# Kernel tuning notes

Hardware: AMD Instinct MI355X
Metric: run time of the kernel (lower is better)

Reference implementation:

```python
import jax, jax.numpy as jnp
import numpy as np

ALPHA = 0.2        # LeakyReLU slope
NEG_BIG = -9e15    # mask fill value from the original module


def setup_inputs() -> dict:
    key = jax.random.key(0)
    k1, k2, k3, k4 = jax.random.split(key, 4)
    N, F_IN, F_OUT = 8192, 256, 128
    h = jax.random.normal(k1, (N, F_IN), dtype=jnp.float32)
    adj = jax.random.randint(k2, (N, N), 0, 2, dtype=jnp.int32)
    W = jax.random.normal(k3, (F_IN, F_OUT), dtype=jnp.float32) * (1.0 / np.sqrt(F_IN))
    a = jax.random.normal(k4, (2 * F_OUT, 1), dtype=jnp.float32) * (1.0 / np.sqrt(2 * F_OUT))
    return {"h": h, "adj": adj, "W": W, "a": a}


def reference(h, adj, W, a):
    f_out = W.shape[1]
    Wh = h @ W                                   # [N, F_out]
    Wh1 = Wh @ a[:f_out, :]                      # [N, 1]
    Wh2 = Wh @ a[f_out:, :]                      # [N, 1]
    e = Wh1 + Wh2.T                              # [N, N] broadcast-add
    e = jnp.where(e > 0, e, ALPHA * e)           # LeakyReLU
    e = jnp.where(adj > 0, e, NEG_BIG)           # adjacency mask
    attention = jax.nn.softmax(e, axis=-1)       # row softmax
    # dropout rate = 0.0 -> identity
    h_prime = attention @ Wh                     # [N, F_out]
    return jax.nn.elu(h_prime)
```

## Files before the change

### kernel.cpp

```cpp
#include <hip/hip_runtime.h>

#define NV 8192
#define FIN 256
#define FOUT 128
#define NSPLIT 8
#define SPLITW 1024

typedef __bf16 bf16_t;
typedef __attribute__((ext_vector_type(8))) __bf16 bf16x8;
typedef __attribute__((ext_vector_type(16))) float f32x16;

__global__ __launch_bounds__(256) void wh_kernel(
    const float* __restrict__ h, const float* __restrict__ W,
    const float* __restrict__ a,
    bf16_t* __restrict__ WhbT,
    float* __restrict__ E1, float* __restrict__ F1,
    float* __restrict__ E2, float* __restrict__ F2)
{
  __shared__ float As[64][34];
  __shared__ float Bs[64][128];
  __shared__ float Cs[32][129];
  __shared__ float red1[32][16];
  __shared__ float red2[32][16];
  const int t  = threadIdx.x;
  const int i0 = blockIdx.x * 32;
  const int c  = t & 15;
  const int r  = t >> 4;
  float acc0[8], acc1[8];
  #pragma unroll
  for (int j = 0; j < 8; j++) { acc0[j] = 0.f; acc1[j] = 0.f; }

  for (int k0 = 0; k0 < FIN; k0 += 64) {
    {
      const int ia = t >> 3;
      const int ka = (t & 7) * 8;
      const float* src = h + (size_t)(i0 + ia) * FIN + k0 + ka;
      float4 v0 = *(const float4*)src;
      float4 v1 = *(const float4*)(src + 4);
      As[ka+0][ia]=v0.x; As[ka+1][ia]=v0.y; As[ka+2][ia]=v0.z; As[ka+3][ia]=v0.w;
      As[ka+4][ia]=v1.x; As[ka+5][ia]=v1.y; As[ka+6][ia]=v1.z; As[ka+7][ia]=v1.w;
    }
    {
      const int kb = t >> 2;
      const int cb = (t & 3) * 32;
      const float4* src = (const float4*)(W + (size_t)(k0 + kb) * FOUT + cb);
      float4* dst = (float4*)&Bs[kb][cb];
      #pragma unroll
      for (int q = 0; q < 8; q++) dst[q] = src[q];
    }
    __syncthreads();
    #pragma unroll 4
    for (int k = 0; k < 64; k++) {
      float2 av = *(const float2*)&As[k][r*2];
      float b[8];
      *(float4*)&b[0] = *(const float4*)&Bs[k][c*8];
      *(float4*)&b[4] = *(const float4*)&Bs[k][c*8+4];
      #pragma unroll
      for (int j = 0; j < 8; j++) {
        acc0[j] = fmaf(av.x, b[j], acc0[j]);
        acc1[j] = fmaf(av.y, b[j], acc1[j]);
      }
    }
    __syncthreads();
  }

  float p1a = 0.f, p2a = 0.f, p1b = 0.f, p2b = 0.f;
  #pragma unroll
  for (int j = 0; j < 8; j++) {
    Cs[r*2][c*8+j]   = acc0[j];
    Cs[r*2+1][c*8+j] = acc1[j];
    float w1 = a[c*8+j];
    float w2 = a[FOUT + c*8+j];
    p1a = fmaf(acc0[j], w1, p1a); p2a = fmaf(acc0[j], w2, p2a);
    p1b = fmaf(acc1[j], w1, p1b); p2b = fmaf(acc1[j], w2, p2b);
  }
  red1[r*2][c]   = p1a; red2[r*2][c]   = p2a;
  red1[r*2+1][c] = p1b; red2[r*2+1][c] = p2b;
  __syncthreads();
  if (t < 32) {
    float s = 0.f;
    #pragma unroll
    for (int q = 0; q < 16; q++) s += red1[t][q];
    E1[i0 + t] = __expf(s);
    F1[i0 + t] = __expf(0.2f * s);
  } else if (t < 64) {
    float s = 0.f;
    #pragma unroll
    for (int q = 0; q < 16; q++) s += red2[t-32][q];
    E2[i0 + t - 32] = __expf(s);
    F2[i0 + t - 32] = __expf(0.2f * s);
  }
  {
    const int f = t & 127, half = t >> 7;
    union { bf16_t b[16]; uint4 v[2]; } pk;
    #pragma unroll
    for (int q = 0; q < 16; q++) pk.b[q] = (bf16_t)Cs[half*16 + q][f];
    uint4* dst = (uint4*)(WhbT + (size_t)f * NV + i0 + half*16);
    dst[0] = pk.v[0]; dst[1] = pk.v[1];
  }
}

__global__ __launch_bounds__(256, 4) void attn_kernel(
    const int* __restrict__ adj, const bf16_t* __restrict__ WhbT,
    const float* __restrict__ E1v, const float* __restrict__ F1v,
    const float* __restrict__ E2v, const float* __restrict__ F2v,
    float* __restrict__ nump, float* __restrict__ denp)
{
  __shared__ bf16_t Plds[64][72];
  __shared__ bf16_t Blds[128][72];
  __shared__ float denlds[64][4];
  const int t     = threadIdx.x;
  const int rb    = blockIdx.x >> 3;
  const int split = blockIdx.x & 7;
  const int i0 = rb * 64;
  const int j0 = split * SPLITW;
  const int il = t >> 2;
  const int jg = (t & 3) * 16;
  const float e1 = E1v[i0 + il];
  const float f1 = F1v[i0 + il];
  const int lane = t & 63;
  const int w    = t >> 6;
  const int rh = (w & 1) * 32;
  const int ch = (w >> 1) * 64;
  const int ml = lane & 31;
  const int kh = (lane >> 5) * 8;
  f32x16 acc0 = {};
  f32x16 acc1 = {};
  float den_t = 0.f;

  const int* arow = adj + (size_t)(i0 + il) * NV + j0 + jg;
  int4 ca0 = *(const int4*)(arow + 0);
  int4 ca1 = *(const int4*)(arow + 4);
  int4 ca2 = *(const int4*)(arow + 8);
  int4 ca3 = *(const int4*)(arow + 12);

  for (int jc = 0; jc < SPLITW; jc += 64) {
    const int jb = j0 + jc;
    const int jn = (jc + 64 < SPLITW) ? jc + 64 : jc;
    const int* nrow = arow + jn;
    int4 na0 = *(const int4*)(nrow + 0);
    int4 na1 = *(const int4*)(nrow + 4);
    int4 na2 = *(const int4*)(nrow + 8);
    int4 na3 = *(const int4*)(nrow + 12);
    {
      const int n  = t >> 1;
      const int hf = (t & 1) * 32;
      const uint4* s4 = (const uint4*)(WhbT + (size_t)n * NV + jb + hf);
      uint4* dst = (uint4*)&Blds[n][hf];
      dst[0] = s4[0]; dst[1] = s4[1]; dst[2] = s4[2]; dst[3] = s4[3];
    }
    {
      const float* e2p = E2v + jb + jg;
      const float* f2p = F2v + jb + jg;
      union { bf16_t b[16]; bf16x8 v[2]; } pk;
      float d0 = 0.f, d1 = 0.f, d2 = 0.f, d3 = 0.f;
      #define PGRP(CA, GG, DD) { \
        float4 e4 = *(const float4*)(e2p + 4*GG); \
        float4 f4 = *(const float4*)(f2p + 4*GG); \
        float px = fmaxf(e1*e4.x, f1*f4.x); px = (CA.x > 0) ? px : 0.f; DD += px; pk.b[4*GG+0] = (bf16_t)px; \
        float py = fmaxf(e1*e4.y, f1*f4.y); py = (CA.y > 0) ? py : 0.f; DD += py; pk.b[4*GG+1] = (bf16_t)py; \
        float pz = fmaxf(e1*e4.z, f1*f4.z); pz = (CA.z > 0) ? pz : 0.f; DD += pz; pk.b[4*GG+2] = (bf16_t)pz; \
        float pw = fmaxf(e1*e4.w, f1*f4.w); pw = (CA.w > 0) ? pw : 0.f; DD += pw; pk.b[4*GG+3] = (bf16_t)pw; }
      PGRP(ca0, 0, d0)
      PGRP(ca1, 1, d1)
      PGRP(ca2, 2, d2)
      PGRP(ca3, 3, d3)
      #undef PGRP
      den_t += (d0 + d1) + (d2 + d3);
      *(bf16x8*)&Plds[il][jg]     = pk.v[0];
      *(bf16x8*)&Plds[il][jg + 8] = pk.v[1];
    }
    asm volatile("s_waitcnt lgkmcnt(0)\n\ts_barrier" ::: "memory");
    #pragma unroll
    for (int ks = 0; ks < 4; ks++) {
      const int k = ks * 16 + kh;
      bf16x8 af = *(const bf16x8*)&Plds[rh + ml][k];
      bf16x8 b0 = *(const bf16x8*)&Blds[ch + ml][k];
      bf16x8 b1 = *(const bf16x8*)&Blds[ch + 32 + ml][k];
      acc0 = __builtin_amdgcn_mfma_f32_32x32x16_bf16(af, b0, acc0, 0, 0, 0);
      acc1 = __builtin_amdgcn_mfma_f32_32x32x16_bf16(af, b1, acc1, 0, 0, 0);
    }
    __syncthreads();
    ca0 = na0; ca1 = na1; ca2 = na2; ca3 = na3;
  }

  denlds[il][t & 3] = den_t;
  __syncthreads();
  if (t < 64) {
    denp[(size_t)split * NV + i0 + t] =
        denlds[t][0] + denlds[t][1] + denlds[t][2] + denlds[t][3];
  }
  float* base = nump + ((size_t)split * NV + i0) * FOUT;
  const int col = ch + ml;
  const int r4  = 4 * (lane >> 5);
  #pragma unroll
  for (int reg = 0; reg < 16; reg++) {
    const int row = rh + (reg & 3) + 8 * (reg >> 2) + r4;
    base[(size_t)row * FOUT + col]      = acc0[reg];
    base[(size_t)row * FOUT + col + 32] = acc1[reg];
  }
}

__global__ __launch_bounds__(256) void finalize_kernel(
    const float* __restrict__ nump, const float* __restrict__ denp,
    float* __restrict__ out)
{
  const int gid = blockIdx.x * 256 + threadIdx.x;
  const int i  = gid >> 5;
  const int f0 = (gid & 31) * 4;
  float den = 0.f;
  #pragma unroll
  for (int sp = 0; sp < NSPLIT; sp++) den += denp[(size_t)sp * NV + i];
  float4 s = make_float4(0.f, 0.f, 0.f, 0.f);
  #pragma unroll
  for (int sp = 0; sp < NSPLIT; sp++) {
    float4 v = *(const float4*)&nump[((size_t)sp * NV + i) * FOUT + f0];
    s.x += v.x; s.y += v.y; s.z += v.z; s.w += v.w;
  }
  const float inv = 1.0f / den;
  float4 r;
  r.x = s.x * inv; r.y = s.y * inv; r.z = s.z * inv; r.w = s.w * inv;
  r.x = r.x > 0.f ? r.x : __expf(r.x) - 1.0f;
  r.y = r.y > 0.f ? r.y : __expf(r.y) - 1.0f;
  r.z = r.z > 0.f ? r.z : __expf(r.z) - 1.0f;
  r.w = r.w > 0.f ? r.w : __expf(r.w) - 1.0f;
  *(float4*)&out[(size_t)i * FOUT + f0] = r;
}

extern "C" void kernel_launch(void* const* d_in, const int* in_sizes, int n_in,
                              void* d_out, int out_size, void* d_ws, size_t ws_size,
                              hipStream_t stream) {
  const float* h  = (const float*)d_in[0];
  const int*  adj = (const int*)d_in[1];
  const float* W  = (const float*)d_in[2];
  const float* a  = (const float*)d_in[3];
  float* out = (float*)d_out;
  char* ws = (char*)d_ws;
  bf16_t* WhbT = (bf16_t*)ws;
  float* E1   = (float*)(ws + 2097152);
  float* F1   = (float*)(ws + 2129920);
  float* E2   = (float*)(ws + 2162688);
  float* F2   = (float*)(ws + 2195456);
  float* denp = (float*)(ws + 2228224);
  float* nump = (float*)(ws + 2490368);

  wh_kernel<<<256, 256, 0, stream>>>(h, W, a, WhbT, E1, F1, E2, F2);
  attn_kernel<<<1024, 256, 0, stream>>>(adj, WhbT, E1, F1, E2, F2, nump, denp);
  finalize_kernel<<<1024, 256, 0, stream>>>(nump, denp, out);
}
```

Before: 414.0 us.

## Prefetch Wh tile into registers and double-buffer its shared-memory copy

The attention kernel now loads the next chunk's WhbT slice into registers during the current iteration and writes it into one of two shared-memory buffers, so the global load latency overlaps the MFMA work. The E2/F2 loads are hoisted ahead of the compute, and the trailing __syncthreads is replaced by a bare s_barrier. The extra buffer raises shared-memory use and register pressure, so the occupancy hint drops from 4 to 3 blocks per CU. Dropping the full waitcnt before the barrier relies on the double buffer to stay correct.

```diff
diff --git a/kernel.cpp b/kernel.cpp
--- a/kernel.cpp
+++ b/kernel.cpp
@@ -100,14 +100,14 @@
   }
 }
 
-__global__ __launch_bounds__(256, 4) void attn_kernel(
+__global__ __launch_bounds__(256, 3) void attn_kernel(
     const int* __restrict__ adj, const bf16_t* __restrict__ WhbT,
     const float* __restrict__ E1v, const float* __restrict__ F1v,
     const float* __restrict__ E2v, const float* __restrict__ F2v,
     float* __restrict__ nump, float* __restrict__ denp)
 {
   __shared__ bf16_t Plds[64][72];
-  __shared__ bf16_t Blds[128][72];
+  __shared__ bf16_t Blds[2][128][72];
   __shared__ float denlds[64][4];
   const int t     = threadIdx.x;
   const int rb    = blockIdx.x >> 3;
@@ -128,59 +128,74 @@
   f32x16 acc1 = {};
   float den_t = 0.f;
 
+  const int bn  = t >> 1;
+  const int bhf = (t & 1) * 32;
+  const bf16_t* bsrc = WhbT + (size_t)bn * NV + j0 + bhf;
   const int* arow = adj + (size_t)(i0 + il) * NV + j0 + jg;
+
+  uint4 br0, br1, br2, br3;
+  {
+    const uint4* s4 = (const uint4*)bsrc;
+    br0 = s4[0]; br1 = s4[1]; br2 = s4[2]; br3 = s4[3];
+  }
   int4 ca0 = *(const int4*)(arow + 0);
   int4 ca1 = *(const int4*)(arow + 4);
   int4 ca2 = *(const int4*)(arow + 8);
   int4 ca3 = *(const int4*)(arow + 12);
 
   for (int jc = 0; jc < SPLITW; jc += 64) {
-    const int jb = j0 + jc;
+    const int jb  = j0 + jc;
+    const int buf = (jc >> 6) & 1;
+    {
+      uint4* bd = (uint4*)&Blds[buf][bn][bhf];
+      bd[0] = br0; bd[1] = br1; bd[2] = br2; bd[3] = br3;
+    }
+    float4 w0 = *(const float4*)(E2v + jb + jg);
+    float4 w1 = *(const float4*)(E2v + jb + jg + 4);
+    float4 w2 = *(const float4*)(E2v + jb + jg + 8);
+    float4 w3 = *(const float4*)(E2v + jb + jg + 12);
+    float4 x0 = *(const float4*)(F2v + jb + jg);
+    float4 x1 = *(const float4*)(F2v + jb + jg + 4);
+    float4 x2 = *(const float4*)(F2v + jb + jg + 8);
+    float4 x3 = *(const float4*)(F2v + jb + jg + 12);
     const int jn = (jc + 64 < SPLITW) ? jc + 64 : jc;
+    {
+      const uint4* s4 = (const uint4*)(bsrc + jn);
+      br0 = s4[0]; br1 = s4[1]; br2 = s4[2]; br3 = s4[3];
+    }
     const int* nrow = arow + jn;
     int4 na0 = *(const int4*)(nrow + 0);
     int4 na1 = *(const int4*)(nrow + 4);
     int4 na2 = *(const int4*)(nrow + 8);
     int4 na3 = *(const int4*)(nrow + 12);
     {
-      const int n  = t >> 1;
-      const int hf = (t & 1) * 32;
-      const uint4* s4 = (const uint4*)(WhbT + (size_t)n * NV + jb + hf);
-      uint4* dst = (uint4*)&Blds[n][hf];
-      dst[0] = s4[0]; dst[1] = s4[1]; dst[2] = s4[2]; dst[3] = s4[3];
-    }
-    {
-      const float* e2p = E2v + jb + jg;
-      const float* f2p = F2v + jb + jg;
-      union { bf16_t b[16]; bf16x8 v[2]; } pk;
+      bf16x8 pv0, pv1;
       float d0 = 0.f, d1 = 0.f, d2 = 0.f, d3 = 0.f;
-      #define PGRP(CA, GG, DD) { \
-        float4 e4 = *(const float4*)(e2p + 4*GG); \
-        float4 f4 = *(const float4*)(f2p + 4*GG); \
-        float px = fmaxf(e1*e4.x, f1*f4.x); px = (CA.x > 0) ? px : 0.f; DD += px; pk.b[4*GG+0] = (bf16_t)px; \
-        float py = fmaxf(e1*e4.y, f1*f4.y); py = (CA.y > 0) ? py : 0.f; DD += py; pk.b[4*GG+1] = (bf16_t)py; \
-        float pz = fmaxf(e1*e4.z, f1*f4.z); pz = (CA.z > 0) ? pz : 0.f; DD += pz; pk.b[4*GG+2] = (bf16_t)pz; \
-        float pw = fmaxf(e1*e4.w, f1*f4.w); pw = (CA.w > 0) ? pw : 0.f; DD += pw; pk.b[4*GG+3] = (bf16_t)pw; }
-      PGRP(ca0, 0, d0)
-      PGRP(ca1, 1, d1)
-      PGRP(ca2, 2, d2)
-      PGRP(ca3, 3, d3)
+      #define PGRP(CA, E4, F4, DD, PV, SL) { \
+        float px = fmaxf(e1*E4.x, f1*F4.x); px = (CA.x > 0) ? px : 0.f; DD += px; PV[SL+0] = (bf16_t)px; \
+        float py = fmaxf(e1*E4.y, f1*F4.y); py = (CA.y > 0) ? py : 0.f; DD += py; PV[SL+1] = (bf16_t)py; \
+        float pz = fmaxf(e1*E4.z, f1*F4.z); pz = (CA.z > 0) ? pz : 0.f; DD += pz; PV[SL+2] = (bf16_t)pz; \
+        float pw = fmaxf(e1*E4.w, f1*F4.w); pw = (CA.w > 0) ? pw : 0.f; DD += pw; PV[SL+3] = (bf16_t)pw; }
+      PGRP(ca0, w0, x0, d0, pv0, 0)
+      PGRP(ca1, w1, x1, d1, pv0, 4)
+      PGRP(ca2, w2, x2, d2, pv1, 0)
+      PGRP(ca3, w3, x3, d3, pv1, 4)
       #undef PGRP
       den_t += (d0 + d1) + (d2 + d3);
-      *(bf16x8*)&Plds[il][jg]     = pk.v[0];
-      *(bf16x8*)&Plds[il][jg + 8] = pk.v[1];
+      *(bf16x8*)&Plds[il][jg]     = pv0;
+      *(bf16x8*)&Plds[il][jg + 8] = pv1;
     }
     asm volatile("s_waitcnt lgkmcnt(0)\n\ts_barrier" ::: "memory");
     #pragma unroll
     for (int ks = 0; ks < 4; ks++) {
       const int k = ks * 16 + kh;
       bf16x8 af = *(const bf16x8*)&Plds[rh + ml][k];
-      bf16x8 b0 = *(const bf16x8*)&Blds[ch + ml][k];
-      bf16x8 b1 = *(const bf16x8*)&Blds[ch + 32 + ml][k];
+      bf16x8 b0 = *(const bf16x8*)&Blds[buf][ch + ml][k];
+      bf16x8 b1 = *(const bf16x8*)&Blds[buf][ch + 32 + ml][k];
       acc0 = __builtin_amdgcn_mfma_f32_32x32x16_bf16(af, b0, acc0, 0, 0, 0);
       acc1 = __builtin_amdgcn_mfma_f32_32x32x16_bf16(af, b1, acc1, 0, 0, 0);
     }
-    __syncthreads();
+    asm volatile("s_barrier" ::: "memory");
     ca0 = na0; ca1 = na1; ca2 = na2; ca3 = na3;
   }
 
```

Measured after the change: 417.6 us. About the same (+0.9%).
